# Optimization experiments

Measured on AMD Instinct MI355X. Metric: run time of the kernel, lower is better.

Reference implementation:

```python
import jax, jax.numpy as jnp
import numpy as np

B, C, H_IMG, W_IMG = 8, 256, 224, 224
PH, PW = 14, 14
NUM_HEADS = 8
HEAD_DIM = C // NUM_HEADS


def setup_inputs() -> dict:
    key = jax.random.key(0)
    ks = jax.random.split(key, 8)
    s = 1.0 / np.sqrt(C)
    return {
        "backbone_features": jax.random.normal(ks[0], (B, C, H_IMG, W_IMG), jnp.float32),
        "query": jax.random.normal(ks[1], (1, 1, C), jnp.float32),
        "in_proj_w": jax.random.uniform(ks[2], (3 * C, C), jnp.float32, -s, s),
        "in_proj_b": jnp.zeros((3 * C,), jnp.float32),
        "attn_out_w": jax.random.uniform(ks[3], (C, C), jnp.float32, -s, s),
        "attn_out_b": jnp.zeros((C,), jnp.float32),
        "out_w": jax.random.uniform(ks[4], (C, C), jnp.float32, -s, s),
        "out_b": jax.random.uniform(ks[5], (C,), jnp.float32, -s, s),
    }


def reference(backbone_features, query, in_proj_w, in_proj_b,
              attn_out_w, attn_out_b, out_w, out_b):
    b, c, h, w = backbone_features.shape
    hp, wp = h // PH, w // PW
    # unfold(2, PH, PH).unfold(3, PW, PW) -> (B, C, Hp, Wp, ph, pw)
    patches = backbone_features.reshape(b, c, hp, PH, wp, PW).transpose(0, 1, 2, 4, 3, 5)
    # (N, L, C) with N = B*Hp*Wp, L = ph*pw
    patch_seq = patches.transpose(0, 2, 3, 4, 5, 1).reshape(b * hp * wp, PH * PW, c)

    wq, wk, wv = in_proj_w[:c], in_proj_w[c:2 * c], in_proj_w[2 * c:]
    bq, bk, bv = in_proj_b[:c], in_proj_b[c:2 * c], in_proj_b[2 * c:]

    # single shared query: project once -> (H, hd)
    qh = (query[0, 0] @ wq.T + bq).reshape(NUM_HEADS, HEAD_DIM)
    k = (patch_seq @ wk.T + bk).reshape(-1, PH * PW, NUM_HEADS, HEAD_DIM)
    v = (patch_seq @ wv.T + bv).reshape(-1, PH * PW, NUM_HEADS, HEAD_DIM)

    scale = 1.0 / np.sqrt(HEAD_DIM)
    scores = jnp.einsum("hd,nlhd->nhl", qh, k) * scale  # (N, H, L)
    attn = jax.nn.softmax(scores, axis=-1)
    ctx = jnp.einsum("nhl,nlhd->nhd", attn, v).reshape(-1, c)  # (N, C)

    attn_out = ctx @ attn_out_w.T + attn_out_b
    pooled = attn_out @ out_w.T + out_b  # (N, C)
    return pooled.reshape(b, hp, wp, c).transpose(0, 3, 1, 2)
```

## Files before the change

kernel.cpp:

```cpp
#include <hip/hip_runtime.h>

#define HW_IMG (224*224)
#define SCALE 0.17677669529663687f

typedef short bf16x8 __attribute__((ext_vector_type(8)));
typedef float f32x4 __attribute__((ext_vector_type(4)));
union U4B8 { uint4 u; bf16x8 b; };

__device__ __forceinline__ unsigned bf16rn(float f) {
  unsigned u = __float_as_uint(f);
  return (u + 0x7fffu + ((u >> 16) & 1u)) >> 16;
}

__global__ void prep1_kernel(const float* __restrict__ query,
                             const float* __restrict__ in_w,
                             const float* __restrict__ in_b,
                             const float* __restrict__ out_w,
                             const float* __restrict__ aob,
                             const float* __restrict__ out_b,
                             float* __restrict__ qh,
                             float* __restrict__ cb) {
  const int r = blockIdx.x, tid = threadIdx.x;
  float p1 = query[tid] * in_w[r*256 + tid];
  float p2 = aob[tid]   * out_w[r*256 + tid];
  #pragma unroll
  for (int o = 32; o; o >>= 1) { p1 += __shfl_xor(p1, o); p2 += __shfl_xor(p2, o); }
  __shared__ float t1[4], t2[4];
  if ((tid & 63) == 0) { t1[tid>>6] = p1; t2[tid>>6] = p2; }
  __syncthreads();
  if (tid == 0) qh[r] = in_b[r] + t1[0]+t1[1]+t1[2]+t1[3];
  if (tid == 1) cb[r] = out_b[r] + t2[0]+t2[1]+t2[2]+t2[3];
}

__global__ void prep2_kernel(const float* __restrict__ qh,
                             const float* __restrict__ in_w,
                             unsigned short* __restrict__ qkf) {
  const int k = blockIdx.x;
  const int L = threadIdx.x;
  const int h = L & 15, q = L >> 4;
  unsigned short o[8];
  #pragma unroll
  for (int j = 0; j < 8; ++j) {
    float s = 0.f;
    if (h < 8) {
      const int c = k*32 + q*8 + j;
      #pragma unroll
      for (int dd = 0; dd < 32; ++dd)
        s += qh[h*32 + dd] * in_w[(256 + h*32 + dd)*256 + c];
      s *= SCALE;
    }
    o[j] = (unsigned short)bf16rn(s);
  }
  ushort4* dst = (ushort4*)(qkf + (size_t)(k*64 + L)*8);
  dst[0] = make_ushort4(o[0],o[1],o[2],o[3]);
  dst[1] = make_ushort4(o[4],o[5],o[6],o[7]);
}

__global__ void prep3_kernel(const float* __restrict__ in_w,
                             const float* __restrict__ aw,
                             const float* __restrict__ out_w,
                             float* __restrict__ wvT,
                             float* __restrict__ cwT) {
  const int o = blockIdx.x, t = threadIdx.x;
  wvT[t*256 + o] = in_w[(512 + o)*256 + t];
  float a = 0.f;
  #pragma unroll 4
  for (int k = 0; k < 256; ++k) a += out_w[o*256 + k] * aw[k*256 + t];
  cwT[t*256 + o] = a;
}

__global__ void transpose_out(const float* __restrict__ pout, float* __restrict__ out) {
  __shared__ float T[64*65];
  const int b  = blockIdx.x;
  const int pc = blockIdx.y;
  const int cc = blockIdx.z;
  const int tid = threadIdx.x;
  const int lc = tid & 63, lr = tid >> 6;
  #pragma unroll
  for (int i = 0; i < 16; ++i) {
    const int p = i*4 + lr;
    T[p*65 + lc] = pout[((size_t)b*256 + pc*64 + p)*256 + cc*64 + lc];
  }
  __syncthreads();
  #pragma unroll
  for (int i = 0; i < 16; ++i) {
    const int c = i*4 + lr;
    out[((size_t)b*256 + cc*64 + c)*256 + pc*64 + lc] = T[lc*65 + c];
  }
}

__global__ __launch_bounds__(256)
__attribute__((amdgpu_waves_per_eu(2, 8)))
void attnpool_main(
    const float* __restrict__ X,
    const float* __restrict__ in_b,
    const unsigned short* __restrict__ qkf,
    const float* __restrict__ wvT,
    const float* __restrict__ cwT,
    const float* __restrict__ cb,
    float* __restrict__ pout,
    float* __restrict__ out) {
  __shared__ float Xs[32*160];
  __shared__ uint4 QKs[8][64];
  __shared__ float Wl[28*8];
  __shared__ float Ms[32], Ss[32];
  __shared__ float SCs[8], Ds[8];

  const int tid = threadIdx.x;
  const int wid = tid >> 6;
  const int lane = tid & 63;
  const int bid = blockIdx.x;
  const int n = (bid & 7) * 256 + (bid >> 3);
  const int b = n >> 8, rem = n & 255, pi = rem >> 4, pj = rem & 15;
  const float* __restrict__ xb = X + (size_t)b*256*HW_IMG + pi*14*224 + pj*14;

  for (int z = tid; z < 640; z += 256) Xs[28*160 + z] = 0.f;

  {
    const uint4* qp = (const uint4*)qkf;
    ((uint4*)QKs)[tid]       = qp[tid];
    ((uint4*)QKs)[256 + tid] = qp[256 + tid];
  }

  int goff[7], w0[7];
  #pragma unroll
  for (int u = 0; u < 7; ++u) {
    const int e = u*256 + tid;
    const int cp = e / 14, p = e - cp*14;
    const int lr = p / 7, j = p - lr*7;
    goff[u] = (2*cp)*HW_IMG + lr*224 + 2*j;
    w0[u] = (2*p)*160 + cp + 4*(p & 7);
  }

  float2 va[7], vb[7];
  #pragma unroll
  for (int u = 0; u < 7; ++u) {
    va[u] = *(const float2*)(xb + goff[u]);
    vb[u] = *(const float2*)(xb + goff[u] + HW_IMG);
  }

  const int arow = wid*16 + (lane & 15);
  const int abase = arow*640 + (lane>>4)*16 + ((arow>>1)&7)*16;
  const int hcol = lane & 15;

  const int o = lane & 31, half = lane >> 5;
  const int pbase = o*16 + half*640;

  float m = -INFINITY, d = 0.f;
  float a0[8] = {0,0,0,0,0,0,0,0}, a1[8] = {0,0,0,0,0,0,0,0};

  #pragma unroll 1
  for (int t = 0; t < 7; ++t) {
    __syncthreads();
    #pragma unroll
    for (int u = 0; u < 7; ++u) {
      ((unsigned*)Xs)[w0[u]]       = bf16rn(va[u].x) | (bf16rn(vb[u].x) << 16);
      ((unsigned*)Xs)[w0[u] + 160] = bf16rn(va[u].y) | (bf16rn(vb[u].y) << 16);
    }
    __syncthreads();
    if (t < 6) {
      const float* xt = xb + (t+1)*448;
      #pragma unroll
      for (int u = 0; u < 7; ++u) {
        va[u] = *(const float2*)(xt + goff[u]);
        vb[u] = *(const float2*)(xt + goff[u] + HW_IMG);
      }
    }
    float s0 = 0.f, s1 = 0.f, s2 = 0.f, s3 = 0.f;
    if (wid < 2) {
      f32x4 sc = {0.f, 0.f, 0.f, 0.f};
      #pragma unroll
      for (int k = 0; k < 8; ++k) {
        U4B8 a;  a.u  = *(const uint4*)((const char*)Xs + abase + k*64);
        U4B8 bq; bq.u = QKs[k][lane];
        sc = __builtin_amdgcn_mfma_f32_16x16x32_bf16(a.b, bq.b, sc, 0, 0, 0);
      }
      const bool pad = (wid == 1) && ((lane>>4) == 3);
      s0 = pad ? -INFINITY : sc[0];
      s1 = pad ? -INFINITY : sc[1];
      s2 = pad ? -INFINITY : sc[2];
      s3 = pad ? -INFINITY : sc[3];
      float mx = fmaxf(fmaxf(s0, s1), fmaxf(s2, s3));
      mx = fmaxf(mx, __shfl_xor(mx, 16));
      mx = fmaxf(mx, __shfl_xor(mx, 32));
      if (lane < 16) Ms[wid*16 + lane] = mx;
    }
    __syncthreads();
    if (wid < 2) {
      const float tm = fmaxf(Ms[hcol], Ms[16 + hcol]);
      const float mn = fmaxf(m, tm);
      const float scl = __expf(m - mn);
      m = mn;
      s0 = __expf(s0 - mn); s1 = __expf(s1 - mn);
      s2 = __expf(s2 - mn); s3 = __expf(s3 - mn);
      float ts = s0 + s1 + s2 + s3;
      ts += __shfl_xor(ts, 16); ts += __shfl_xor(ts, 32);
      if (lane < 16) Ss[wid*16 + lane] = ts;
      if (wid == 0 && lane < 8) SCs[lane] = scl;
      const int rbase = wid*16 + (lane>>4)*4;
      if (hcol < 8 && rbase < 28) {
        Wl[(rbase+0)*8 + hcol] = s0;
        Wl[(rbase+1)*8 + hcol] = s1;
        Wl[(rbase+2)*8 + hcol] = s2;
        Wl[(rbase+3)*8 + hcol] = s3;
      }
      d *= scl;
    }
    __syncthreads();
    if (wid < 2) d += Ss[hcol] + Ss[16 + hcol];
    {
      const float sa = SCs[2*wid], sb = SCs[2*wid + 1];
      #pragma unroll
      for (int nn = 0; nn < 8; ++nn) { a0[nn] *= sa; a1[nn] *= sb; }
      #pragma unroll
      for (int i = 0; i < 14; ++i) {
        const int r = 2*i + half;
        const uint4 xv = *(const uint4*)((const char*)Xs + pbase + i*1280 + (i&7)*16);
        const float2 w2 = *(const float2*)&Wl[r*8 + 2*wid];
        #pragma unroll
        for (int nn = 0; nn < 4; ++nn) {
          const unsigned uu = ((const unsigned*)&xv)[nn];
          const float xl = __uint_as_float(uu << 16);
          const float xh = __uint_as_float(uu & 0xffff0000u);
          a0[2*nn]   += w2.x * xl; a0[2*nn+1] += w2.x * xh;
          a1[2*nn]   += w2.y * xl; a1[2*nn+1] += w2.y * xh;
        }
      }
    }
  }

  if (wid == 0 && lane < 8) Ds[lane] = d;
  __syncthreads();
  {
    #pragma unroll
    for (int nn = 0; nn < 8; ++nn) {
      a0[nn] += __shfl_xor(a0[nn], 32);
      a1[nn] += __shfl_xor(a1[nn], 32);
    }
    if (half == 0) {
      const float i0 = 1.f / Ds[2*wid], i1 = 1.f / Ds[2*wid + 1];
      #pragma unroll
      for (int nn = 0; nn < 8; ++nn) { a0[nn] *= i0; a1[nn] *= i1; }
      f32x4 t0 = {a0[0], a0[1], a0[2], a0[3]};
      f32x4 t1 = {a0[4], a0[5], a0[6], a0[7]};
      f32x4 t2 = {a1[0], a1[1], a1[2], a1[3]};
      f32x4 t3 = {a1[4], a1[5], a1[6], a1[7]};
      *(f32x4*)&Xs[(2*wid)*256 + 8*o]       = t0;
      *(f32x4*)&Xs[(2*wid)*256 + 8*o + 4]   = t1;
      *(f32x4*)&Xs[(2*wid+1)*256 + 8*o]     = t2;
      *(f32x4*)&Xs[(2*wid+1)*256 + 8*o + 4] = t3;
    }
  }
  __syncthreads();
  {
    const int h2 = tid >> 5;
    float a = in_b[512 + tid];
    #pragma unroll 8
    for (int c = 0; c < 256; ++c) a += wvT[c*256 + tid] * Xs[h2*256 + c];
    Xs[2048 + tid] = a;
  }
  __syncthreads();
  {
    float oo = cb[tid];
    #pragma unroll 8
    for (int k = 0; k < 256; ++k) oo += cwT[k*256 + tid] * Xs[2048 + k];
    if (pout) pout[(size_t)n*256 + tid] = oo;
    else out[(((size_t)b*256 + tid)*16 + pi)*16 + pj] = oo;
  }
}

extern "C" void kernel_launch(void* const* d_in, const int* in_sizes, int n_in,
                              void* d_out, int out_size, void* d_ws, size_t ws_size,
                              hipStream_t stream) {
  const float* X    = (const float*)d_in[0];
  const float* q    = (const float*)d_in[1];
  const float* in_w = (const float*)d_in[2];
  const float* in_b = (const float*)d_in[3];
  const float* aw   = (const float*)d_in[4];
  const float* aob  = (const float*)d_in[5];
  const float* ow   = (const float*)d_in[6];
  const float* ob   = (const float*)d_in[7];
  float* out = (float*)d_out;

  float* wsf = (float*)d_ws;
  float* qh   = wsf;
  float* cb   = wsf + 256;
  unsigned short* qkf = (unsigned short*)(wsf + 512);
  float* wvT  = wsf + 4096;
  float* cwT  = wsf + 4096 + 65536;
  const size_t need = (size_t)(4096 + 2*65536 + 2048*256) * sizeof(float);
  float* pout = (ws_size >= need) ? (wsf + 4096 + 2*65536) : nullptr;

  hipLaunchKernelGGL(prep1_kernel, dim3(256),  dim3(256), 0, stream,
                     q, in_w, in_b, ow, aob, ob, qh, cb);
  hipLaunchKernelGGL(prep2_kernel, dim3(8),    dim3(64),  0, stream,
                     qh, in_w, qkf);
  hipLaunchKernelGGL(prep3_kernel, dim3(256),  dim3(256), 0, stream,
                     in_w, aw, ow, wvT, cwT);
  hipLaunchKernelGGL(attnpool_main, dim3(2048), dim3(256), 0, stream,
                     X, in_b, qkf, wvT, cwT, cb, pout, out);
  if (pout)
    hipLaunchKernelGGL(transpose_out, dim3(8, 4, 4), dim3(256), 0, stream,
                       pout, out);
}
```

Before: 236.1 us.

## Warp-specialize loader waves with double-buffered LDS and per-wave softmax rescaling

Splits the block so waves 2-3 act as producers that load, convert to bf16 and commit the next patch-row tile into a second LDS buffer, while waves 0-1 compute scores on the current buffer. The online softmax now computes exponentials against a per-wave local max and rescales them by factors derived from both waves' maxima, which removes the extra barrier and the shared sum and scale arrays. Each iteration now has two barriers instead of three. In exchange, LDS use doubles, producer waves hold more registers (28 staged words), and the global-load work is concentrated in half the waves.

```diff
diff --git a/kernel.cpp b/kernel.cpp
--- a/kernel.cpp
+++ b/kernel.cpp
@@ -100,11 +100,10 @@
     const float* __restrict__ cb,
     float* __restrict__ pout,
     float* __restrict__ out) {
-  __shared__ float Xs[32*160];
+  __shared__ float Xs[2][32*160];
   __shared__ uint4 QKs[8][64];
-  __shared__ float Wl[28*8];
-  __shared__ float Ms[32], Ss[32];
-  __shared__ float SCs[8], Ds[8];
+  __shared__ float Wl[32*8];
+  __shared__ float Ms[2][8];
 
   const int tid = threadIdx.x;
   const int wid = tid >> 6;
@@ -114,141 +113,156 @@
   const int b = n >> 8, rem = n & 255, pi = rem >> 4, pj = rem & 15;
   const float* __restrict__ xb = X + (size_t)b*256*HW_IMG + pi*14*224 + pj*14;
 
-  for (int z = tid; z < 640; z += 256) Xs[28*160 + z] = 0.f;
-
+  for (int z = tid; z < 640; z += 256) {
+    Xs[0][28*160 + z] = 0.f;
+    Xs[1][28*160 + z] = 0.f;
+  }
   {
     const uint4* qp = (const uint4*)qkf;
     ((uint4*)QKs)[tid]       = qp[tid];
     ((uint4*)QKs)[256 + tid] = qp[256 + tid];
   }
 
-  int goff[7], w0[7];
-  #pragma unroll
-  for (int u = 0; u < 7; ++u) {
-    const int e = u*256 + tid;
-    const int cp = e / 14, p = e - cp*14;
-    const int lr = p / 7, j = p - lr*7;
-    goff[u] = (2*cp)*HW_IMG + lr*224 + 2*j;
-    w0[u] = (2*p)*160 + cp + 4*(p & 7);
-  }
-
-  float2 va[7], vb[7];
-  #pragma unroll
-  for (int u = 0; u < 7; ++u) {
-    va[u] = *(const float2*)(xb + goff[u]);
-    vb[u] = *(const float2*)(xb + goff[u] + HW_IMG);
-  }
+  int goff[14], w0s[14];
+  unsigned st[28];
+  const int lt = tid - 128;
+  if (wid >= 2) {
+    #pragma unroll
+    for (int u = 0; u < 14; ++u) {
+      const int e = u*128 + lt;
+      const int cp = e / 14, p = e - cp*14;
+      const int lr = p / 7, j = p - lr*7;
+      goff[u] = (2*cp)*HW_IMG + lr*224 + 2*j;
+      w0s[u]  = (2*p)*160 + cp + 4*(p & 7);
+    }
+  }
+  auto stage = [&](int t) {
+    const float* xt = xb + t*448;
+    float2 va[14], vb[14];
+    #pragma unroll
+    for (int u = 0; u < 14; ++u) {
+      va[u] = *(const float2*)(xt + goff[u]);
+      vb[u] = *(const float2*)(xt + goff[u] + HW_IMG);
+    }
+    #pragma unroll
+    for (int u = 0; u < 14; ++u) {
+      st[2*u]   = bf16rn(va[u].x) | (bf16rn(vb[u].x) << 16);
+      st[2*u+1] = bf16rn(va[u].y) | (bf16rn(vb[u].y) << 16);
+    }
+  };
+  auto commit = [&](float* dst) {
+    #pragma unroll
+    for (int u = 0; u < 14; ++u) {
+      ((unsigned*)dst)[w0s[u]]       = st[2*u];
+      ((unsigned*)dst)[w0s[u] + 160] = st[2*u+1];
+    }
+  };
 
   const int arow = wid*16 + (lane & 15);
   const int abase = arow*640 + (lane>>4)*16 + ((arow>>1)&7)*16;
   const int hcol = lane & 15;
+  const int rbase = wid*16 + (lane>>4)*4;
 
   const int o = lane & 31, half = lane >> 5;
   const int pbase = o*16 + half*640;
-
-  float m = -INFINITY, d = 0.f;
+  const int hA = 2*wid, hB = hA + 1;
+
+  float mA = -INFINITY, mB = -INFINITY, dA = 0.f, dB = 0.f;
   float a0[8] = {0,0,0,0,0,0,0,0}, a1[8] = {0,0,0,0,0,0,0,0};
 
+  if (wid >= 2) { stage(0); commit(Xs[0]); stage(1); }
+  __syncthreads();
+
+  int cur = 0;
   #pragma unroll 1
   for (int t = 0; t < 7; ++t) {
-    __syncthreads();
-    #pragma unroll
-    for (int u = 0; u < 7; ++u) {
-      ((unsigned*)Xs)[w0[u]]       = bf16rn(va[u].x) | (bf16rn(vb[u].x) << 16);
-      ((unsigned*)Xs)[w0[u] + 160] = bf16rn(va[u].y) | (bf16rn(vb[u].y) << 16);
-    }
-    __syncthreads();
-    if (t < 6) {
-      const float* xt = xb + (t+1)*448;
-      #pragma unroll
-      for (int u = 0; u < 7; ++u) {
-        va[u] = *(const float2*)(xt + goff[u]);
-        vb[u] = *(const float2*)(xt + goff[u] + HW_IMG);
-      }
-    }
-    float s0 = 0.f, s1 = 0.f, s2 = 0.f, s3 = 0.f;
     if (wid < 2) {
       f32x4 sc = {0.f, 0.f, 0.f, 0.f};
+      const char* xc = (const char*)&Xs[cur][0];
       #pragma unroll
       for (int k = 0; k < 8; ++k) {
-        U4B8 a;  a.u  = *(const uint4*)((const char*)Xs + abase + k*64);
+        U4B8 a;  a.u  = *(const uint4*)(xc + abase + k*64);
         U4B8 bq; bq.u = QKs[k][lane];
         sc = __builtin_amdgcn_mfma_f32_16x16x32_bf16(a.b, bq.b, sc, 0, 0, 0);
       }
       const bool pad = (wid == 1) && ((lane>>4) == 3);
-      s0 = pad ? -INFINITY : sc[0];
-      s1 = pad ? -INFINITY : sc[1];
-      s2 = pad ? -INFINITY : sc[2];
-      s3 = pad ? -INFINITY : sc[3];
+      const float s0 = pad ? -INFINITY : sc[0];
+      const float s1 = pad ? -INFINITY : sc[1];
+      const float s2 = pad ? -INFINITY : sc[2];
+      const float s3 = pad ? -INFINITY : sc[3];
       float mx = fmaxf(fmaxf(s0, s1), fmaxf(s2, s3));
       mx = fmaxf(mx, __shfl_xor(mx, 16));
       mx = fmaxf(mx, __shfl_xor(mx, 32));
-      if (lane < 16) Ms[wid*16 + lane] = mx;
+      const float e0 = __expf(s0 - mx), e1 = __expf(s1 - mx);
+      const float e2 = __expf(s2 - mx), e3 = __expf(s3 - mx);
+      if (hcol < 8) {
+        if (lane < 8) Ms[wid][lane] = mx;
+        if (rbase < 28) {
+          Wl[(rbase+0)*8 + hcol] = e0;
+          Wl[(rbase+1)*8 + hcol] = e1;
+          Wl[(rbase+2)*8 + hcol] = e2;
+          Wl[(rbase+3)*8 + hcol] = e3;
+        }
+      }
+    } else {
+      if (t < 6) commit(&Xs[cur^1][0]);
     }
     __syncthreads();
-    if (wid < 2) {
-      const float tm = fmaxf(Ms[hcol], Ms[16 + hcol]);
-      const float mn = fmaxf(m, tm);
-      const float scl = __expf(m - mn);
-      m = mn;
-      s0 = __expf(s0 - mn); s1 = __expf(s1 - mn);
-      s2 = __expf(s2 - mn); s3 = __expf(s3 - mn);
-      float ts = s0 + s1 + s2 + s3;
-      ts += __shfl_xor(ts, 16); ts += __shfl_xor(ts, 32);
-      if (lane < 16) Ss[wid*16 + lane] = ts;
-      if (wid == 0 && lane < 8) SCs[lane] = scl;
-      const int rbase = wid*16 + (lane>>4)*4;
-      if (hcol < 8 && rbase < 28) {
-        Wl[(rbase+0)*8 + hcol] = s0;
-        Wl[(rbase+1)*8 + hcol] = s1;
-        Wl[(rbase+2)*8 + hcol] = s2;
-        Wl[(rbase+3)*8 + hcol] = s3;
-      }
-      d *= scl;
-    }
-    __syncthreads();
-    if (wid < 2) d += Ss[hcol] + Ss[16 + hcol];
+
     {
-      const float sa = SCs[2*wid], sb = SCs[2*wid + 1];
+      const float m0A = Ms[0][hA], m1A = Ms[1][hA];
+      const float m0B = Ms[0][hB], m1B = Ms[1][hB];
+      const float mnA = fmaxf(fmaxf(m0A, m1A), mA);
+      const float mnB = fmaxf(fmaxf(m0B, m1B), mB);
+      const float sA = __expf(mA - mnA), sB = __expf(mB - mnB);
+      const float fA0 = __expf(m0A - mnA), fA1 = __expf(m1A - mnA);
+      const float fB0 = __expf(m0B - mnB), fB1 = __expf(m1B - mnB);
+      mA = mnA; mB = mnB;
+      dA *= sA; dB *= sB;
       #pragma unroll
-      for (int nn = 0; nn < 8; ++nn) { a0[nn] *= sa; a1[nn] *= sb; }
+      for (int nn = 0; nn < 8; ++nn) { a0[nn] *= sA; a1[nn] *= sB; }
+      const char* xc = (const char*)&Xs[cur][0];
       #pragma unroll
       for (int i = 0; i < 14; ++i) {
         const int r = 2*i + half;
-        const uint4 xv = *(const uint4*)((const char*)Xs + pbase + i*1280 + (i&7)*16);
-        const float2 w2 = *(const float2*)&Wl[r*8 + 2*wid];
+        const uint4 xv = *(const uint4*)(xc + pbase + i*1280 + (i&7)*16);
+        const float2 w2 = *(const float2*)&Wl[r*8 + hA];
+        const float wA = w2.x * (i < 8 ? fA0 : fA1);
+        const float wB = w2.y * (i < 8 ? fB0 : fB1);
+        dA += wA; dB += wB;
         #pragma unroll
         for (int nn = 0; nn < 4; ++nn) {
           const unsigned uu = ((const unsigned*)&xv)[nn];
           const float xl = __uint_as_float(uu << 16);
           const float xh = __uint_as_float(uu & 0xffff0000u);
-          a0[2*nn]   += w2.x * xl; a0[2*nn+1] += w2.x * xh;
-          a1[2*nn]   += w2.y * xl; a1[2*nn+1] += w2.y * xh;
+          a0[2*nn]   += wA * xl; a0[2*nn+1] += wA * xh;
+          a1[2*nn]   += wB * xl; a1[2*nn+1] += wB * xh;
         }
       }
     }
-  }
-
-  if (wid == 0 && lane < 8) Ds[lane] = d;
-  __syncthreads();
+    if (wid >= 2 && t < 5) stage(t+2);
+    __syncthreads();
+    cur ^= 1;
+  }
+
   {
     #pragma unroll
     for (int nn = 0; nn < 8; ++nn) {
       a0[nn] += __shfl_xor(a0[nn], 32);
       a1[nn] += __shfl_xor(a1[nn], 32);
     }
+    dA += __shfl_xor(dA, 32);
+    dB += __shfl_xor(dB, 32);
     if (half == 0) {
-      const float i0 = 1.f / Ds[2*wid], i1 = 1.f / Ds[2*wid + 1];
-      #pragma unroll
-      for (int nn = 0; nn < 8; ++nn) { a0[nn] *= i0; a1[nn] *= i1; }
-      f32x4 t0 = {a0[0], a0[1], a0[2], a0[3]};
-      f32x4 t1 = {a0[4], a0[5], a0[6], a0[7]};
-      f32x4 t2 = {a1[0], a1[1], a1[2], a1[3]};
-      f32x4 t3 = {a1[4], a1[5], a1[6], a1[7]};
-      *(f32x4*)&Xs[(2*wid)*256 + 8*o]       = t0;
-      *(f32x4*)&Xs[(2*wid)*256 + 8*o + 4]   = t1;
-      *(f32x4*)&Xs[(2*wid+1)*256 + 8*o]     = t2;
-      *(f32x4*)&Xs[(2*wid+1)*256 + 8*o + 4] = t3;
+      const float iA = 1.f / dA, iB = 1.f / dB;
+      f32x4 t0 = {a0[0]*iA, a0[1]*iA, a0[2]*iA, a0[3]*iA};
+      f32x4 t1 = {a0[4]*iA, a0[5]*iA, a0[6]*iA, a0[7]*iA};
+      f32x4 t2 = {a1[0]*iB, a1[1]*iB, a1[2]*iB, a1[3]*iB};
+      f32x4 t3 = {a1[4]*iB, a1[5]*iB, a1[6]*iB, a1[7]*iB};
+      *(f32x4*)&Xs[0][hA*256 + 8*o]     = t0;
+      *(f32x4*)&Xs[0][hA*256 + 8*o + 4] = t1;
+      *(f32x4*)&Xs[0][hB*256 + 8*o]     = t2;
+      *(f32x4*)&Xs[0][hB*256 + 8*o + 4] = t3;
     }
   }
   __syncthreads();
@@ -256,14 +270,14 @@
     const int h2 = tid >> 5;
     float a = in_b[512 + tid];
     #pragma unroll 8
-    for (int c = 0; c < 256; ++c) a += wvT[c*256 + tid] * Xs[h2*256 + c];
-    Xs[2048 + tid] = a;
+    for (int c = 0; c < 256; ++c) a += wvT[c*256 + tid] * Xs[0][h2*256 + c];
+    Xs[0][2048 + tid] = a;
   }
   __syncthreads();
   {
     float oo = cb[tid];
     #pragma unroll 8
-    for (int k = 0; k < 256; ++k) oo += cwT[k*256 + tid] * Xs[2048 + k];
+    for (int k = 0; k < 256; ++k) oo += cwT[k*256 + tid] * Xs[0][2048 + k];
     if (pout) pout[(size_t)n*256 + tid] = oo;
     else out[(((size_t)b*256 + tid)*16 + pi)*16 + pj] = oo;
   }
```

New measurement: 250.2 us. 6.0% more time.

## Add repack pass converting input to patch-major bf16 before main kernel

Applied to the files above, without the earlier changes.

A new repack kernel reads the NCHW fp32 input with coalesced float4 loads, transposes it through shared memory, and writes a patch-contiguous bf16 buffer. The main attention kernel then fetches its tiles with wide 16-byte loads instead of strided float2 gathers and per-element bf16 conversion. The aim is to remove uncoalesced global access and conversion work from the main kernel. The cost is an extra pass that reads the full input and writes a half-size copy. The workspace-size check is also dropped, so pout and Y are now used unconditionally.

```diff
diff --git a/kernel.cpp b/kernel.cpp
--- a/kernel.cpp
+++ b/kernel.cpp
@@ -10,6 +10,9 @@
 __device__ __forceinline__ unsigned bf16rn(float f) {
   unsigned u = __float_as_uint(f);
   return (u + 0x7fffu + ((u >> 16) & 1u)) >> 16;
+}
+__device__ __forceinline__ unsigned packbf(float a, float b) {
+  return bf16rn(a) | (bf16rn(b) << 16);
 }
 
 __global__ void prep1_kernel(const float* __restrict__ query,
@@ -69,6 +72,48 @@
   cwT[t*256 + o] = a;
 }
 
+__global__ __launch_bounds__(256) void repack_kernel(
+    const float* __restrict__ X, unsigned short* __restrict__ Y) {
+  __shared__ float T[64*68];
+  const int bx = blockIdx.x;
+  const int g = (bx & 7)*448 + (bx >> 3);
+  const int cg = g & 3;
+  const int rest = g >> 2;
+  const int R = rest % 112, b = rest / 112;
+  const int pi = R / 7, rr = R % 7;
+  const int tid = threadIdx.x;
+  const float* xbase = X + ((size_t)b*256 + cg*64)*HW_IMG + (pi*14 + rr*2)*224;
+  const int cq = tid & 15, posg = tid >> 4;
+  const size_t nb = ((size_t)b*16 + pi)*16;
+
+  #pragma unroll 1
+  for (int tt = 0; tt < 7; ++tt) {
+    #pragma unroll
+    for (int k = 0; k < 4; ++k) {
+      const int u = tid + 256*k;
+      const int c = u >> 4, f = u & 15;
+      const float4 v = *(const float4*)(xbase + (size_t)c*HW_IMG + tt*64 + f*4);
+      *(float4*)&T[c*68 + f*4] = v;
+    }
+    __syncthreads();
+    #pragma unroll
+    for (int k = 0; k < 4; ++k) {
+      const int pl = posg + 16*k;
+      const int p = tt*64 + pl;
+      const int imgrow = p / 224, col = p - imgrow*224;
+      const int pj = col / 14, jj = col - pj*14;
+      const int l = rr*28 + imgrow*14 + jj;
+      const float v0 = T[(4*cq+0)*68 + pl];
+      const float v1 = T[(4*cq+1)*68 + pl];
+      const float v2 = T[(4*cq+2)*68 + pl];
+      const float v3 = T[(4*cq+3)*68 + pl];
+      uint2 w; w.x = packbf(v0, v1); w.y = packbf(v2, v3);
+      *(uint2*)(Y + ((((nb + pj)*4 + cg)*196 + l)*64 + cq*4)) = w;
+    }
+    __syncthreads();
+  }
+}
+
 __global__ void transpose_out(const float* __restrict__ pout, float* __restrict__ out) {
   __shared__ float T[64*65];
   const int b  = blockIdx.x;
@@ -92,7 +137,7 @@
 __global__ __launch_bounds__(256)
 __attribute__((amdgpu_waves_per_eu(2, 8)))
 void attnpool_main(
-    const float* __restrict__ X,
+    const unsigned short* __restrict__ Y,
     const float* __restrict__ in_b,
     const unsigned short* __restrict__ qkf,
     const float* __restrict__ wvT,
@@ -102,7 +147,7 @@
     float* __restrict__ out) {
   __shared__ float Xs[32*160];
   __shared__ uint4 QKs[8][64];
-  __shared__ float Wl[28*8];
+  __shared__ float Wl[32*8];
   __shared__ float Ms[32], Ss[32];
   __shared__ float SCs[8], Ds[8];
 
@@ -112,36 +157,44 @@
   const int bid = blockIdx.x;
   const int n = (bid & 7) * 256 + (bid >> 3);
   const int b = n >> 8, rem = n & 255, pi = rem >> 4, pj = rem & 15;
-  const float* __restrict__ xb = X + (size_t)b*256*HW_IMG + pi*14*224 + pj*14;
 
   for (int z = tid; z < 640; z += 256) Xs[28*160 + z] = 0.f;
-
   {
     const uint4* qp = (const uint4*)qkf;
     ((uint4*)QKs)[tid]       = qp[tid];
     ((uint4*)QKs)[256 + tid] = qp[256 + tid];
   }
 
-  int goff[7], w0[7];
-  #pragma unroll
-  for (int u = 0; u < 7; ++u) {
-    const int e = u*256 + tid;
-    const int cp = e / 14, p = e - cp*14;
-    const int lr = p / 7, j = p - lr*7;
-    goff[u] = (2*cp)*HW_IMG + lr*224 + 2*j;
-    w0[u] = (2*p)*160 + cp + 4*(p & 7);
-  }
-
-  float2 va[7], vb[7];
-  #pragma unroll
-  for (int u = 0; u < 7; ++u) {
-    va[u] = *(const float2*)(xb + goff[u]);
-    vb[u] = *(const float2*)(xb + goff[u] + HW_IMG);
-  }
+  const unsigned short* Yn = Y + (size_t)n * (4*196*64);
+  int soff[4], dstw[4];
+  #pragma unroll
+  for (int k = 0; k < 4; ++k) {
+    const int u = tid + 256*k;
+    const int uu = (u < 896) ? u : 0;
+    const int cgk = uu / 224, rm = uu - cgk*224;
+    const int lo = rm >> 3, c8 = rm & 7;
+    soff[k] = (cgk*196 + lo)*64 + c8*8;
+    dstw[k] = lo*160 + cgk*32 + c8*4 + 4*((lo>>1)&7);
+  }
+  uint4 pf[4];
+  auto fetchT = [&](int t) {
+    const unsigned short* yt = Yn + t*1792;
+    pf[0] = *(const uint4*)(yt + soff[0]);
+    pf[1] = *(const uint4*)(yt + soff[1]);
+    pf[2] = *(const uint4*)(yt + soff[2]);
+    if (tid < 128) pf[3] = *(const uint4*)(yt + soff[3]);
+  };
+  auto commitT = [&]() {
+    *(uint4*)&((unsigned*)Xs)[dstw[0]] = pf[0];
+    *(uint4*)&((unsigned*)Xs)[dstw[1]] = pf[1];
+    *(uint4*)&((unsigned*)Xs)[dstw[2]] = pf[2];
+    if (tid < 128) *(uint4*)&((unsigned*)Xs)[dstw[3]] = pf[3];
+  };
 
   const int arow = wid*16 + (lane & 15);
   const int abase = arow*640 + (lane>>4)*16 + ((arow>>1)&7)*16;
   const int hcol = lane & 15;
+  const int rbase = wid*16 + (lane>>4)*4;
 
   const int o = lane & 31, half = lane >> 5;
   const int pbase = o*16 + half*640;
@@ -149,23 +202,14 @@
   float m = -INFINITY, d = 0.f;
   float a0[8] = {0,0,0,0,0,0,0,0}, a1[8] = {0,0,0,0,0,0,0,0};
 
+  fetchT(0);
   #pragma unroll 1
   for (int t = 0; t < 7; ++t) {
     __syncthreads();
-    #pragma unroll
-    for (int u = 0; u < 7; ++u) {
-      ((unsigned*)Xs)[w0[u]]       = bf16rn(va[u].x) | (bf16rn(vb[u].x) << 16);
-      ((unsigned*)Xs)[w0[u] + 160] = bf16rn(va[u].y) | (bf16rn(vb[u].y) << 16);
-    }
-    __syncthreads();
-    if (t < 6) {
-      const float* xt = xb + (t+1)*448;
-      #pragma unroll
-      for (int u = 0; u < 7; ++u) {
-        va[u] = *(const float2*)(xt + goff[u]);
-        vb[u] = *(const float2*)(xt + goff[u] + HW_IMG);
-      }
-    }
+    commitT();
+    __syncthreads();
+    if (t < 6) fetchT(t+1);
+
     float s0 = 0.f, s1 = 0.f, s2 = 0.f, s3 = 0.f;
     if (wid < 2) {
       f32x4 sc = {0.f, 0.f, 0.f, 0.f};
@@ -197,7 +241,6 @@
       ts += __shfl_xor(ts, 16); ts += __shfl_xor(ts, 32);
       if (lane < 16) Ss[wid*16 + lane] = ts;
       if (wid == 0 && lane < 8) SCs[lane] = scl;
-      const int rbase = wid*16 + (lane>>4)*4;
       if (hcol < 8 && rbase < 28) {
         Wl[(rbase+0)*8 + hcol] = s0;
         Wl[(rbase+1)*8 + hcol] = s1;
@@ -288,8 +331,8 @@
   unsigned short* qkf = (unsigned short*)(wsf + 512);
   float* wvT  = wsf + 4096;
   float* cwT  = wsf + 4096 + 65536;
-  const size_t need = (size_t)(4096 + 2*65536 + 2048*256) * sizeof(float);
-  float* pout = (ws_size >= need) ? (wsf + 4096 + 2*65536) : nullptr;
+  float* pout = wsf + 4096 + 2*65536;
+  unsigned short* Y = (unsigned short*)(wsf + 4096 + 2*65536 + 524288);
 
   hipLaunchKernelGGL(prep1_kernel, dim3(256),  dim3(256), 0, stream,
                      q, in_w, in_b, ow, aob, ob, qh, cb);
@@ -297,9 +340,10 @@
                      qh, in_w, qkf);
   hipLaunchKernelGGL(prep3_kernel, dim3(256),  dim3(256), 0, stream,
                      in_w, aw, ow, wvT, cwT);
+  hipLaunchKernelGGL(repack_kernel, dim3(3584), dim3(256), 0, stream,
+                     X, Y);
   hipLaunchKernelGGL(attnpool_main, dim3(2048), dim3(256), 0, stream,
-                     X, in_b, qkf, wvT, cwT, cb, pout, out);
-  if (pout)
-    hipLaunchKernelGGL(transpose_out, dim3(8, 4, 4), dim3(256), 0, stream,
-                       pout, out);
-}
+                     Y, in_b, qkf, wvT, cwT, cb, pout, out);
+  hipLaunchKernelGGL(transpose_out, dim3(8, 4, 4), dim3(256), 0, stream,
+                     pout, out);
+}
```

After: 323.6 us. +37.1%, slower.

## Split fused attention-pool kernel into repack/score, pool, and batched projection stages

Applied to the files above, without the earlier changes.

Replaces the single per-patch fused kernel with three stages. The first reads X with row-contiguous loads per channel group, writes a bf16 repacked copy of each patch and partial scores per channel quarter. The second sums the partial scores, applies the softmax and does the weighted pooling with MFMA. The third runs the V and output projections for 8 patches per block so weight reads are shared across patches. This targets the strided gathers and the per-patch weight traffic of the old kernel, at the cost of writing and re-reading a large bf16 intermediate plus fp32 partial scores through global memory.

```diff
diff --git a/kernel.cpp b/kernel.cpp
--- a/kernel.cpp
+++ b/kernel.cpp
@@ -10,6 +10,9 @@
 __device__ __forceinline__ unsigned bf16rn(float f) {
   unsigned u = __float_as_uint(f);
   return (u + 0x7fffu + ((u >> 16) & 1u)) >> 16;
+}
+__device__ __forceinline__ unsigned packbf(float a, float b) {
+  return bf16rn(a) | (bf16rn(b) << 16);
 }
 
 __global__ void prep1_kernel(const float* __restrict__ query,
@@ -34,39 +37,298 @@
 
 __global__ void prep2_kernel(const float* __restrict__ qh,
                              const float* __restrict__ in_w,
-                             unsigned short* __restrict__ qkf) {
-  const int k = blockIdx.x;
-  const int L = threadIdx.x;
-  const int h = L & 15, q = L >> 4;
-  unsigned short o[8];
-  #pragma unroll
-  for (int j = 0; j < 8; ++j) {
-    float s = 0.f;
-    if (h < 8) {
-      const int c = k*32 + q*8 + j;
-      #pragma unroll
-      for (int dd = 0; dd < 32; ++dd)
-        s += qh[h*32 + dd] * in_w[(256 + h*32 + dd)*256 + c];
-      s *= SCALE;
-    }
-    o[j] = (unsigned short)bf16rn(s);
-  }
-  ushort4* dst = (ushort4*)(qkf + (size_t)(k*64 + L)*8);
-  dst[0] = make_ushort4(o[0],o[1],o[2],o[3]);
-  dst[1] = make_ushort4(o[4],o[5],o[6],o[7]);
-}
-
-__global__ void prep3_kernel(const float* __restrict__ in_w,
-                             const float* __restrict__ aw,
+                             unsigned short* __restrict__ qk2g) {
+  const int h = blockIdx.x;
+  const int c = threadIdx.x;
+  float s = 0.f;
+  if (h < 8) {
+    #pragma unroll
+    for (int d = 0; d < 32; ++d)
+      s += qh[h*32 + d] * in_w[(256 + h*32 + d)*256 + c];
+    s *= SCALE;
+  }
+  qk2g[h*256 + c] = (unsigned short)bf16rn(s);
+}
+
+__global__ void prep3_kernel(const float* __restrict__ aw,
                              const float* __restrict__ out_w,
-                             float* __restrict__ wvT,
                              float* __restrict__ cwT) {
   const int o = blockIdx.x, t = threadIdx.x;
-  wvT[t*256 + o] = in_w[(512 + o)*256 + t];
   float a = 0.f;
   #pragma unroll 4
   for (int k = 0; k < 256; ++k) a += out_w[o*256 + k] * aw[k*256 + t];
   cwT[t*256 + o] = a;
+}
+
+__global__ __launch_bounds__(256)
+__attribute__((amdgpu_waves_per_eu(2, 8)))
+void k1_repack_scores(const float* __restrict__ X,
+                      const unsigned short* __restrict__ qk2g,
+                      unsigned short* __restrict__ Yp,
+                      float* __restrict__ Sp) {
+  __shared__ unsigned Tt[400*36];
+  __shared__ float sps[8*404];
+  __shared__ unsigned qk_l[16*36];
+
+  const int tid = threadIdx.x;
+  const int lane = tid & 63;
+  const int wid = tid >> 6;
+  const int bx = blockIdx.x;
+  const int g = (bx & 7)*64 + (bx >> 3);
+  const int cg = g & 3;
+  const int rest = g >> 2;
+  const int pi = rest & 15, b = rest >> 4;
+
+  #pragma unroll
+  for (int i = 0; i < 2; ++i) {
+    const int u = tid + 256*i;
+    const int h = u >> 5, cl2 = u & 31;
+    qk_l[h*36 + cl2] = *(const unsigned*)(qk2g + h*256 + cg*64 + 2*cl2);
+  }
+  __syncthreads();
+
+  U4B8 a0, a1;
+  a0.u = *(const uint4*)&qk_l[(lane & 15)*36 + (lane >> 4)*4];
+  a1.u = *(const uint4*)&qk_l[(lane & 15)*36 + 16 + (lane >> 4)*4];
+
+  const int c2 = tid & 31, q = tid >> 5;
+  const float* xc0 = X + (size_t)(b*256 + cg*64 + 2*c2)*HW_IMG + pi*14*224;
+  const float* xc1 = xc0 + HW_IMG;
+
+  #pragma unroll 1
+  for (int ct = 0; ct < 8; ++ct) {
+    #pragma unroll
+    for (int r = 0; r < 14; ++r) {
+      #pragma unroll
+      for (int j = 0; j < 2; ++j) {
+        const int f = q + 8*j;
+        if (f < 14) {
+          const int off = r*224 + ct*28 + 2*f;
+          const float2 v0 = *(const float2*)(xc0 + off);
+          const float2 v1 = *(const float2*)(xc1 + off);
+          const int pos = r*28 + 2*f;
+          Tt[pos*36 + c2]     = packbf(v0.x, v1.x);
+          Tt[(pos+1)*36 + c2] = packbf(v0.y, v1.y);
+        }
+      }
+    }
+    __syncthreads();
+
+    for (int ti = wid; ti < 25; ti += 4) {
+      U4B8 b0, b1;
+      const int prow = ti*16 + (lane & 15);
+      b0.u = *(const uint4*)&Tt[prow*36 + (lane >> 4)*4];
+      b1.u = *(const uint4*)&Tt[prow*36 + 16 + (lane >> 4)*4];
+      f32x4 d = {0.f, 0.f, 0.f, 0.f};
+      d = __builtin_amdgcn_mfma_f32_16x16x32_bf16(a0.b, b0.b, d, 0, 0, 0);
+      d = __builtin_amdgcn_mfma_f32_16x16x32_bf16(a1.b, b1.b, d, 0, 0, 0);
+      if ((lane >> 4) < 2) {
+        const int h = (lane >> 4)*4;
+        const int pp = ti*16 + (lane & 15);
+        sps[(h+0)*404 + pp] = d[0];
+        sps[(h+1)*404 + pp] = d[1];
+        sps[(h+2)*404 + pp] = d[2];
+        sps[(h+3)*404 + pp] = d[3];
+      }
+    }
+
+    #pragma unroll
+    for (int k = 0; k < 4; ++k) {
+      const int id = tid + 256*k;
+      if (id < 896) {
+        const int c2l = id & 31, pj2 = (id >> 5) & 1, r = id >> 6;
+        unsigned w[16];
+        #pragma unroll
+        for (int jj = 0; jj < 14; ++jj)
+          w[jj] = Tt[(r*28 + pj2*14 + jj)*36 + c2l];
+        w[14] = 0u; w[15] = 0u;
+        const int n = (b*16 + pi)*16 + ct*2 + pj2;
+        unsigned short* dst = Yp + (size_t)n*57344 + (cg*32 + c2l)*448 + 32*r;
+        *(uint4*)(dst)      = make_uint4(w[0],  w[1],  w[2],  w[3]);
+        *(uint4*)(dst + 8)  = make_uint4(w[4],  w[5],  w[6],  w[7]);
+        *(uint4*)(dst + 16) = make_uint4(w[8],  w[9],  w[10], w[11]);
+        *(uint4*)(dst + 24) = make_uint4(w[12], w[13], w[14], w[15]);
+      }
+    }
+    __syncthreads();
+
+    {
+      const int h = tid & 7, r = (tid >> 3) & 15, pj2 = (tid >> 7) & 1;
+      if (r < 14) {
+        float s[16];
+        #pragma unroll
+        for (int jj = 0; jj < 14; ++jj)
+          s[jj] = sps[h*404 + r*28 + pj2*14 + jj];
+        s[14] = 0.f; s[15] = 0.f;
+        const int n = (b*16 + pi)*16 + ct*2 + pj2;
+        float* dst = Sp + ((size_t)(cg*2048 + n)*8 + h)*224 + 16*r;
+        *(float4*)(dst)      = make_float4(s[0],  s[1],  s[2],  s[3]);
+        *(float4*)(dst + 4)  = make_float4(s[4],  s[5],  s[6],  s[7]);
+        *(float4*)(dst + 8)  = make_float4(s[8],  s[9],  s[10], s[11]);
+        *(float4*)(dst + 12) = make_float4(s[12], s[13], s[14], s[15]);
+      }
+    }
+    __syncthreads();
+  }
+}
+
+__global__ __launch_bounds__(256)
+__attribute__((amdgpu_waves_per_eu(2, 8)))
+void k2_pool(const unsigned short* __restrict__ Yp,
+             const float* __restrict__ Sp,
+             float* __restrict__ pooled) {
+  __shared__ float sm[1792];
+  __shared__ unsigned aw[16*116];
+  __shared__ float pool_s[8*260];
+
+  const int tid = threadIdx.x;
+  const int lane = tid & 63, wid = tid >> 6;
+  const int bid = blockIdx.x;
+  const int n = (bid & 7)*256 + (bid >> 3);
+
+  #pragma unroll
+  for (int i = 0; i < 4; ++i) {
+    const int u = tid + 256*i;
+    if (u < 928) aw[928 + u] = 0u;
+  }
+
+  const float* spn = Sp + (size_t)n*1792;
+  #pragma unroll
+  for (int j = 0; j < 7; ++j) {
+    const int idx = tid + 256*j;
+    sm[idx] = spn[idx] + spn[3670016 + idx] + spn[2*3670016 + idx] + spn[3*3670016 + idx];
+  }
+  __syncthreads();
+
+  {
+    const int h = tid >> 5, l = tid & 31;
+    float sv[7]; bool msk[7];
+    float mx = -1e30f;
+    #pragma unroll
+    for (int j = 0; j < 7; ++j) {
+      const int L = l + 32*j;
+      sv[j] = sm[h*224 + L];
+      msk[j] = (L & 15) < 14;
+      if (msk[j]) mx = fmaxf(mx, sv[j]);
+    }
+    #pragma unroll
+    for (int o = 16; o; o >>= 1) mx = fmaxf(mx, __shfl_xor(mx, o, 32));
+    float d = 0.f;
+    #pragma unroll
+    for (int j = 0; j < 7; ++j) {
+      sv[j] = msk[j] ? __expf(sv[j] - mx) : 0.f;
+      d += sv[j];
+    }
+    #pragma unroll
+    for (int o = 16; o; o >>= 1) d += __shfl_xor(d, o, 32);
+    const float inv = 1.f / d;
+    #pragma unroll
+    for (int j = 0; j < 7; ++j) {
+      const float w = sv[j] * inv;
+      const float wn = __shfl_xor(w, 1, 32);
+      if ((l & 1) == 0) aw[h*116 + ((l + 32*j) >> 1)] = packbf(w, wn);
+    }
+  }
+  __syncthreads();
+
+  U4B8 bfrag[7];
+  #pragma unroll
+  for (int ks = 0; ks < 7; ++ks)
+    bfrag[ks].u = *(const uint4*)&aw[(lane & 15)*116 + ks*16 + (lane >> 4)*4];
+
+  const unsigned short* yn = Yp + (size_t)n*57344;
+  const int mr = lane & 15, kq = lane >> 4;
+  const int par = mr & 1;
+  f32x4 acc[4] = {{0,0,0,0},{0,0,0,0},{0,0,0,0},{0,0,0,0}};
+  #pragma unroll
+  for (int ks = 0; ks < 7; ++ks) {
+    #pragma unroll
+    for (int Mt = 0; Mt < 4; ++Mt) {
+      const int c2g = (wid*64 + Mt*16 + mr) >> 1;
+      const unsigned short* p = yn + c2g*448 + ks*64 + kq*16;
+      const uint4 U = *(const uint4*)p;
+      const uint4 V = *(const uint4*)(p + 8);
+      U4B8 af;
+      if (par == 0) {
+        af.u.x = (U.x & 0xffffu) | (U.y << 16);
+        af.u.y = (U.z & 0xffffu) | (U.w << 16);
+        af.u.z = (V.x & 0xffffu) | (V.y << 16);
+        af.u.w = (V.z & 0xffffu) | (V.w << 16);
+      } else {
+        af.u.x = (U.x >> 16) | (U.y & 0xffff0000u);
+        af.u.y = (U.z >> 16) | (U.w & 0xffff0000u);
+        af.u.z = (V.x >> 16) | (V.y & 0xffff0000u);
+        af.u.w = (V.z >> 16) | (V.w & 0xffff0000u);
+      }
+      acc[Mt] = __builtin_amdgcn_mfma_f32_16x16x32_bf16(af.b, bfrag[ks].b, acc[Mt], 0, 0, 0);
+    }
+  }
+
+  if ((lane & 15) < 8) {
+    const int hh = lane & 15;
+    #pragma unroll
+    for (int Mt = 0; Mt < 4; ++Mt) {
+      const int cc = wid*64 + Mt*16 + (lane >> 4)*4;
+      pool_s[hh*260 + cc + 0] = acc[Mt][0];
+      pool_s[hh*260 + cc + 1] = acc[Mt][1];
+      pool_s[hh*260 + cc + 2] = acc[Mt][2];
+      pool_s[hh*260 + cc + 3] = acc[Mt][3];
+    }
+  }
+  __syncthreads();
+  {
+    const int hh = tid >> 5, cc = (tid & 31)*8;
+    const float4 o0 = *(const float4*)&pool_s[hh*260 + cc];
+    const float4 o1 = *(const float4*)&pool_s[hh*260 + cc + 4];
+    float* dst = pooled + (size_t)n*2048 + tid*8;
+    *(float4*)(dst)     = o0;
+    *(float4*)(dst + 4) = o1;
+  }
+}
+
+__global__ __launch_bounds__(256) void k3_proj(
+    const float* __restrict__ pooled,
+    const float* __restrict__ in_w,
+    const float* __restrict__ in_b,
+    const float* __restrict__ cwT,
+    const float* __restrict__ cb,
+    float* __restrict__ pout) {
+  __shared__ float ctx_s[8*260];
+  const int tid = threadIdx.x;
+  const int bx = blockIdx.x;
+  const int g = (bx & 7)*32 + (bx >> 3);
+  const int n0 = g*8;
+
+  {
+    const int k = tid, hk = k >> 5;
+    const float* wv = in_w + (size_t)(512 + k)*256;
+    float acc[8] = {0,0,0,0,0,0,0,0};
+    for (int c = 0; c < 256; c += 4) {
+      const float4 wf = *(const float4*)(wv + c);
+      #pragma unroll
+      for (int nn = 0; nn < 8; ++nn) {
+        const float4 pf = *(const float4*)(pooled + (size_t)(n0 + nn)*2048 + hk*256 + c);
+        acc[nn] += wf.x*pf.x + wf.y*pf.y + wf.z*pf.z + wf.w*pf.w;
+      }
+    }
+    const float bvk = in_b[512 + k];
+    #pragma unroll
+    for (int nn = 0; nn < 8; ++nn) ctx_s[nn*260 + k] = acc[nn] + bvk;
+  }
+  __syncthreads();
+  {
+    float oo[8];
+    const float cbo = cb[tid];
+    #pragma unroll
+    for (int nn = 0; nn < 8; ++nn) oo[nn] = cbo;
+    for (int kk = 0; kk < 256; ++kk) {
+      const float cwv = cwT[kk*256 + tid];
+      #pragma unroll
+      for (int nn = 0; nn < 8; ++nn) oo[nn] += cwv * ctx_s[nn*260 + kk];
+    }
+    #pragma unroll
+    for (int nn = 0; nn < 8; ++nn) pout[(size_t)(n0 + nn)*256 + tid] = oo[nn];
+  }
 }
 
 __global__ void transpose_out(const float* __restrict__ pout, float* __restrict__ out) {
@@ -86,186 +348,6 @@
   for (int i = 0; i < 16; ++i) {
     const int c = i*4 + lr;
     out[((size_t)b*256 + cc*64 + c)*256 + pc*64 + lc] = T[lc*65 + c];
-  }
-}
-
-__global__ __launch_bounds__(256)
-__attribute__((amdgpu_waves_per_eu(2, 8)))
-void attnpool_main(
-    const float* __restrict__ X,
-    const float* __restrict__ in_b,
-    const unsigned short* __restrict__ qkf,
-    const float* __restrict__ wvT,
-    const float* __restrict__ cwT,
-    const float* __restrict__ cb,
-    float* __restrict__ pout,
-    float* __restrict__ out) {
-  __shared__ float Xs[32*160];
-  __shared__ uint4 QKs[8][64];
-  __shared__ float Wl[28*8];
-  __shared__ float Ms[32], Ss[32];
-  __shared__ float SCs[8], Ds[8];
-
-  const int tid = threadIdx.x;
-  const int wid = tid >> 6;
-  const int lane = tid & 63;
-  const int bid = blockIdx.x;
-  const int n = (bid & 7) * 256 + (bid >> 3);
-  const int b = n >> 8, rem = n & 255, pi = rem >> 4, pj = rem & 15;
-  const float* __restrict__ xb = X + (size_t)b*256*HW_IMG + pi*14*224 + pj*14;
-
-  for (int z = tid; z < 640; z += 256) Xs[28*160 + z] = 0.f;
-
-  {
-    const uint4* qp = (const uint4*)qkf;
-    ((uint4*)QKs)[tid]       = qp[tid];
-    ((uint4*)QKs)[256 + tid] = qp[256 + tid];
-  }
-
-  int goff[7], w0[7];
-  #pragma unroll
-  for (int u = 0; u < 7; ++u) {
-    const int e = u*256 + tid;
-    const int cp = e / 14, p = e - cp*14;
-    const int lr = p / 7, j = p - lr*7;
-    goff[u] = (2*cp)*HW_IMG + lr*224 + 2*j;
-    w0[u] = (2*p)*160 + cp + 4*(p & 7);
-  }
-
-  float2 va[7], vb[7];
-  #pragma unroll
-  for (int u = 0; u < 7; ++u) {
-    va[u] = *(const float2*)(xb + goff[u]);
-    vb[u] = *(const float2*)(xb + goff[u] + HW_IMG);
-  }
-
-  const int arow = wid*16 + (lane & 15);
-  const int abase = arow*640 + (lane>>4)*16 + ((arow>>1)&7)*16;
-  const int hcol = lane & 15;
-
-  const int o = lane & 31, half = lane >> 5;
-  const int pbase = o*16 + half*640;
-
-  float m = -INFINITY, d = 0.f;
-  float a0[8] = {0,0,0,0,0,0,0,0}, a1[8] = {0,0,0,0,0,0,0,0};
-
-  #pragma unroll 1
-  for (int t = 0; t < 7; ++t) {
-    __syncthreads();
-    #pragma unroll
-    for (int u = 0; u < 7; ++u) {
-      ((unsigned*)Xs)[w0[u]]       = bf16rn(va[u].x) | (bf16rn(vb[u].x) << 16);
-      ((unsigned*)Xs)[w0[u] + 160] = bf16rn(va[u].y) | (bf16rn(vb[u].y) << 16);
-    }
-    __syncthreads();
-    if (t < 6) {
-      const float* xt = xb + (t+1)*448;
-      #pragma unroll
-      for (int u = 0; u < 7; ++u) {
-        va[u] = *(const float2*)(xt + goff[u]);
-        vb[u] = *(const float2*)(xt + goff[u] + HW_IMG);
-      }
-    }
-    float s0 = 0.f, s1 = 0.f, s2 = 0.f, s3 = 0.f;
-    if (wid < 2) {
-      f32x4 sc = {0.f, 0.f, 0.f, 0.f};
-      #pragma unroll
-      for (int k = 0; k < 8; ++k) {
-        U4B8 a;  a.u  = *(const uint4*)((const char*)Xs + abase + k*64);
-        U4B8 bq; bq.u = QKs[k][lane];
-        sc = __builtin_amdgcn_mfma_f32_16x16x32_bf16(a.b, bq.b, sc, 0, 0, 0);
-      }
-      const bool pad = (wid == 1) && ((lane>>4) == 3);
-      s0 = pad ? -INFINITY : sc[0];
-      s1 = pad ? -INFINITY : sc[1];
-      s2 = pad ? -INFINITY : sc[2];
-      s3 = pad ? -INFINITY : sc[3];
-      float mx = fmaxf(fmaxf(s0, s1), fmaxf(s2, s3));
-      mx = fmaxf(mx, __shfl_xor(mx, 16));
-      mx = fmaxf(mx, __shfl_xor(mx, 32));
-      if (lane < 16) Ms[wid*16 + lane] = mx;
-    }
-    __syncthreads();
-    if (wid < 2) {
-      const float tm = fmaxf(Ms[hcol], Ms[16 + hcol]);
-      const float mn = fmaxf(m, tm);
-      const float scl = __expf(m - mn);
-      m = mn;
-      s0 = __expf(s0 - mn); s1 = __expf(s1 - mn);
-      s2 = __expf(s2 - mn); s3 = __expf(s3 - mn);
-      float ts = s0 + s1 + s2 + s3;
-      ts += __shfl_xor(ts, 16); ts += __shfl_xor(ts, 32);
-      if (lane < 16) Ss[wid*16 + lane] = ts;
-      if (wid == 0 && lane < 8) SCs[lane] = scl;
-      const int rbase = wid*16 + (lane>>4)*4;
-      if (hcol < 8 && rbase < 28) {
-        Wl[(rbase+0)*8 + hcol] = s0;
-        Wl[(rbase+1)*8 + hcol] = s1;
-        Wl[(rbase+2)*8 + hcol] = s2;
-        Wl[(rbase+3)*8 + hcol] = s3;
-      }
-      d *= scl;
-    }
-    __syncthreads();
-    if (wid < 2) d += Ss[hcol] + Ss[16 + hcol];
-    {
-      const float sa = SCs[2*wid], sb = SCs[2*wid + 1];
-      #pragma unroll
-      for (int nn = 0; nn < 8; ++nn) { a0[nn] *= sa; a1[nn] *= sb; }
-      #pragma unroll
-      for (int i = 0; i < 14; ++i) {
-        const int r = 2*i + half;
-        const uint4 xv = *(const uint4*)((const char*)Xs + pbase + i*1280 + (i&7)*16);
-        const float2 w2 = *(const float2*)&Wl[r*8 + 2*wid];
-        #pragma unroll
-        for (int nn = 0; nn < 4; ++nn) {
-          const unsigned uu = ((const unsigned*)&xv)[nn];
-          const float xl = __uint_as_float(uu << 16);
-          const float xh = __uint_as_float(uu & 0xffff0000u);
-          a0[2*nn]   += w2.x * xl; a0[2*nn+1] += w2.x * xh;
-          a1[2*nn]   += w2.y * xl; a1[2*nn+1] += w2.y * xh;
-        }
-      }
-    }
-  }
-
-  if (wid == 0 && lane < 8) Ds[lane] = d;
-  __syncthreads();
-  {
-    #pragma unroll
-    for (int nn = 0; nn < 8; ++nn) {
-      a0[nn] += __shfl_xor(a0[nn], 32);
-      a1[nn] += __shfl_xor(a1[nn], 32);
-    }
-    if (half == 0) {
-      const float i0 = 1.f / Ds[2*wid], i1 = 1.f / Ds[2*wid + 1];
-      #pragma unroll
-      for (int nn = 0; nn < 8; ++nn) { a0[nn] *= i0; a1[nn] *= i1; }
-      f32x4 t0 = {a0[0], a0[1], a0[2], a0[3]};
-      f32x4 t1 = {a0[4], a0[5], a0[6], a0[7]};
-      f32x4 t2 = {a1[0], a1[1], a1[2], a1[3]};
-      f32x4 t3 = {a1[4], a1[5], a1[6], a1[7]};
-      *(f32x4*)&Xs[(2*wid)*256 + 8*o]       = t0;
-      *(f32x4*)&Xs[(2*wid)*256 + 8*o + 4]   = t1;
-      *(f32x4*)&Xs[(2*wid+1)*256 + 8*o]     = t2;
-      *(f32x4*)&Xs[(2*wid+1)*256 + 8*o + 4] = t3;
-    }
-  }
-  __syncthreads();
-  {
-    const int h2 = tid >> 5;
-    float a = in_b[512 + tid];
-    #pragma unroll 8
-    for (int c = 0; c < 256; ++c) a += wvT[c*256 + tid] * Xs[h2*256 + c];
-    Xs[2048 + tid] = a;
-  }
-  __syncthreads();
-  {
-    float oo = cb[tid];
-    #pragma unroll 8
-    for (int k = 0; k < 256; ++k) oo += cwT[k*256 + tid] * Xs[2048 + k];
-    if (pout) pout[(size_t)n*256 + tid] = oo;
-    else out[(((size_t)b*256 + tid)*16 + pi)*16 + pj] = oo;
   }
 }
 
@@ -285,21 +367,25 @@
   float* wsf = (float*)d_ws;
   float* qh   = wsf;
   float* cb   = wsf + 256;
-  unsigned short* qkf = (unsigned short*)(wsf + 512);
-  float* wvT  = wsf + 4096;
-  float* cwT  = wsf + 4096 + 65536;
-  const size_t need = (size_t)(4096 + 2*65536 + 2048*256) * sizeof(float);
-  float* pout = (ws_size >= need) ? (wsf + 4096 + 2*65536) : nullptr;
-
-  hipLaunchKernelGGL(prep1_kernel, dim3(256),  dim3(256), 0, stream,
+  unsigned short* qk2g = (unsigned short*)(wsf + 512);
+  float* cwT  = wsf + 4096;
+  float* pout = wsf + 69632;
+  float* pooled = wsf + 593920;
+  float* Sp   = wsf + 4788224;
+  unsigned short* Yp = (unsigned short*)(wsf + 19468288);
+
+  hipLaunchKernelGGL(prep1_kernel, dim3(256), dim3(256), 0, stream,
                      q, in_w, in_b, ow, aob, ob, qh, cb);
-  hipLaunchKernelGGL(prep2_kernel, dim3(8),    dim3(64),  0, stream,
-                     qh, in_w, qkf);
-  hipLaunchKernelGGL(prep3_kernel, dim3(256),  dim3(256), 0, stream,
-                     in_w, aw, ow, wvT, cwT);
-  hipLaunchKernelGGL(attnpool_main, dim3(2048), dim3(256), 0, stream,
-                     X, in_b, qkf, wvT, cwT, cb, pout, out);
-  if (pout)
-    hipLaunchKernelGGL(transpose_out, dim3(8, 4, 4), dim3(256), 0, stream,
-                       pout, out);
-}
+  hipLaunchKernelGGL(prep2_kernel, dim3(16), dim3(256), 0, stream,
+                     qh, in_w, qk2g);
+  hipLaunchKernelGGL(prep3_kernel, dim3(256), dim3(256), 0, stream,
+                     aw, ow, cwT);
+  hipLaunchKernelGGL(k1_repack_scores, dim3(512), dim3(256), 0, stream,
+                     X, qk2g, Yp, Sp);
+  hipLaunchKernelGGL(k2_pool, dim3(2048), dim3(256), 0, stream,
+                     Yp, Sp, pooled);
+  hipLaunchKernelGGL(k3_proj, dim3(256), dim3(256), 0, stream,
+                     pooled, in_w, in_b, cwT, cb, pout);
+  hipLaunchKernelGGL(transpose_out, dim3(8, 4, 4), dim3(256), 0, stream,
+                     pout, out);
+}
```

Result: slower. 445.0 us (+88.5%).
